# Performance work log

Hardware: AMD Instinct MI355X
Metric: run time of the kernel (lower is better)

## Reference

```python
import jax, jax.numpy as jnp
import numpy as np

N_USERS = 100000
N_ITEMS = 50000
N = N_USERS + N_ITEMS
EMB_DIM = 64
N_LAYERS = 3
NNZ = 6400000
BATCH = 4096


def setup_inputs() -> dict:
    key = jax.random.key(0)
    k = jax.random.split(key, 7)
    user_emb = 0.1 * jax.random.normal(k[0], (N_USERS, EMB_DIM), dtype=jnp.float32)
    item_emb = 0.1 * jax.random.normal(k[1], (N_ITEMS, EMB_DIM), dtype=jnp.float32)
    graph_val = jax.random.uniform(k[2], (NNZ,), dtype=jnp.float32) * 0.05
    graph_src = jax.random.randint(k[3], (NNZ,), 0, N, dtype=jnp.int64) if jax.config.jax_enable_x64 else jax.random.randint(k[3], (NNZ,), 0, N).astype(jnp.int32)
    graph_dst = jax.random.randint(k[4], (NNZ,), 0, N).astype(graph_src.dtype)
    users = jax.random.randint(k[5], (BATCH,), 0, N_USERS).astype(graph_src.dtype)
    items = jax.random.randint(k[6], (BATCH,), 0, N_ITEMS).astype(graph_src.dtype)
    return {"user_emb": user_emb, "item_emb": item_emb, "graph_val": graph_val,
            "graph_src": graph_src, "graph_dst": graph_dst, "users": users, "items": items}


def _spmm(val, src, dst, x):
    # y[src] += val * x[dst]  -- sparse (COO) matrix @ dense
    return jax.ops.segment_sum(val[:, None] * x[dst], src, num_segments=N)


def reference(user_emb, item_emb, graph_val, graph_src, graph_dst, users, items):
    all_emb = jnp.concatenate([user_emb, item_emb], axis=0)  # [N, d]
    acc = all_emb  # running sum over layers (fused mean accumulation)
    x = all_emb
    for _ in range(N_LAYERS):
        x = _spmm(graph_val, graph_src, graph_dst, x)
        acc = acc + x
    light_out = acc / (N_LAYERS + 1)
    all_users = light_out[:N_USERS]
    all_items = light_out[N_USERS:]
    scores = jnp.sum(all_users[users] * all_items[items], axis=1)  # [B]
    return scores
```

## Files before the change

kernel.cpp:

```cpp
#include <hip/hip_runtime.h>


constexpr int N_USERS = 100000;
constexpr int N_ITEMS = 50000;
constexpr int N_NODES = N_USERS + N_ITEMS;
constexpr int EMB = 64;
constexpr int NNZ = 6400000;
constexpr int BATCH = 4096;

constexpr int BSHIFT = 9;
constexpr int BWIDTH = 1 << BSHIFT;
constexpr int NB = (N_NODES + BWIDTH - 1) >> BSHIFT;
constexpr int NBPAD = 512;
constexpr int BSTRIDE = 23500;

constexpr int TILE = 5120;
constexpr int P1_BLOCKS = NNZ / TILE;
constexpr int EPT1 = TILE / 256;

constexpr float QSCALE = 327680.0f;
constexpr float QINV   = 1.0f / 327680.0f;

struct h4 { _Float16 x, y, z, w; };
typedef _Float16 half4v __attribute__((ext_vector_type(4)));

__global__ void gcur_init_kernel(int* __restrict__ gcur) {
    int i = blockIdx.x * blockDim.x + threadIdx.x;
    if (i < NB) gcur[i] = i * BSTRIDE;
}

__global__ void p1_bin_kernel(const int* __restrict__ src, const int* __restrict__ dst,
                              const float* __restrict__ val, int* __restrict__ gcur,
                              uint2* __restrict__ staging) {
    __shared__ int hist[NBPAD];
    __shared__ int gbase[NBPAD];
    __shared__ int cur[NBPAD];
    __shared__ int sbuf[NBPAD];
    __shared__ int lbase[NBPAD];
    __shared__ uint2 ebuf[TILE];
    int t = threadIdx.x;
    int tile = blockIdx.x * TILE;
    int srcs[EPT1];
    #pragma unroll
    for (int k = 0; k < EPT1; ++k) srcs[k] = src[tile + t + k * 256];
    for (int i = t; i < NBPAD; i += 256) { hist[i] = 0; cur[i] = 0; }
    __syncthreads();
    #pragma unroll
    for (int k = 0; k < EPT1; ++k) atomicAdd(&hist[srcs[k] >> BSHIFT], 1);
    __syncthreads();
    for (int i = t; i < NB; i += 256) {
        int h = hist[i];
        gbase[i] = (h > 0) ? atomicAdd(&gcur[i], h) : 0;
    }
    for (int i = t; i < NBPAD; i += 256) sbuf[i] = hist[i];
    __syncthreads();
    int* pin = sbuf; int* pout = lbase;
    for (int off = 1; off < NBPAD; off <<= 1) {
        for (int i = t; i < NBPAD; i += 256) {
            int v = pin[i];
            if (i >= off) v += pin[i - off];
            pout[i] = v;
        }
        __syncthreads();
        int* tmp = pin; pin = pout; pout = tmp;
    }
    for (int i = t; i < NBPAD; i += 256) lbase[i] = pin[i] - hist[i];
    __syncthreads();
    #pragma unroll
    for (int k = 0; k < EPT1; ++k) {
        int i = tile + t + k * 256;
        int s = srcs[k];
        int b = s >> BSHIFT;
        int c = atomicAdd(&cur[b], 1);
        int d = dst[i];
        float v = val[i];
        unsigned q = (unsigned)(v * QSCALE);
        if (q > 16383u) q = 16383u;
        ebuf[lbase[b] + c] = make_uint2((q << 18) | (unsigned)d, (unsigned)s);
    }
    __syncthreads();
    #pragma unroll
    for (int k = 0; k < EPT1; ++k) {
        int j = t + k * 256;
        uint2 e = ebuf[j];
        int b = (int)(e.y >> BSHIFT);
        unsigned pos = (unsigned)(gbase[b] + (j - lbase[b]));
        if (pos < (unsigned)((b + 1) * BSTRIDE))
            staging[pos] = e;
    }
}

__global__ void bucket_scan_kernel(const int* __restrict__ gcur, int* __restrict__ fbase,
                                   int* __restrict__ roff) {
    __shared__ int sA[NBPAD], sB[NBPAD];
    int t = threadIdx.x;
    int c = (t < NB) ? (gcur[t] - t * BSTRIDE) : 0;
    if (c > BSTRIDE) c = BSTRIDE;
    sA[t] = c;
    __syncthreads();
    int* pin = sA; int* pout = sB;
    for (int off = 1; off < NBPAD; off <<= 1) {
        int v = pin[t];
        if (t >= off) v += pin[t - off];
        pout[t] = v;
        __syncthreads();
        int* tmp = pin; pin = pout; pout = tmp;
    }
    if (t < NB) fbase[t] = pin[t] - c;
    if (t == NB - 1) roff[N_NODES] = pin[t];
}

__global__ void p2_sort_kernel(const int* __restrict__ gcur, const int* __restrict__ fbase,
                               const uint2* __restrict__ staging, unsigned* __restrict__ epack,
                               int* __restrict__ roff) {
    __shared__ int hist[BWIDTH], sA[BWIDTH], sB[BWIDTH], cur[BWIDTH];
    int b = blockIdx.x;
    int t = threadIdx.x;
    int cnt = gcur[b] - b * BSTRIDE;
    if (cnt > BSTRIDE) cnt = BSTRIDE;
    int fb = fbase[b];
    int sbase = b * BSTRIDE;
    for (int i = t; i < BWIDTH; i += 256) hist[i] = 0;
    __syncthreads();
    for (int j = t; j < cnt; j += 256) {
        uint2 e = staging[sbase + j];
        atomicAdd(&hist[e.y & (BWIDTH - 1)], 1);
    }
    __syncthreads();
    for (int i = t; i < BWIDTH; i += 256) sA[i] = hist[i];
    __syncthreads();
    int* pin = sA; int* pout = sB;
    for (int off = 1; off < BWIDTH; off <<= 1) {
        for (int i = t; i < BWIDTH; i += 256) {
            int v = pin[i];
            if (i >= off) v += pin[i - off];
            pout[i] = v;
        }
        __syncthreads();
        int* tmp = pin; pin = pout; pout = tmp;
    }
    for (int i = t; i < BWIDTH; i += 256) {
        int excl = pin[i] - hist[i];
        cur[i] = excl;
        int node = (b << BSHIFT) + i;
        if (node < N_NODES) roff[node] = fb + excl;
    }
    __syncthreads();
    for (int j = t; j < cnt; j += 256) {
        uint2 e = staging[sbase + j];
        int p = atomicAdd(&cur[e.y & (BWIDTH - 1)], 1);
        epack[fb + p] = e.x;
    }
}

__global__ void init_kernel(const float4* __restrict__ ue, const float4* __restrict__ ie,
                            h4* __restrict__ x) {
    int i = blockIdx.x * blockDim.x + threadIdx.x;
    const int total = N_NODES * (EMB / 4);
    if (i >= total) return;
    const int usplit = N_USERS * (EMB / 4);
    float4 v = (i < usplit) ? ue[i] : ie[i - usplit];
    x[i] = h4{(_Float16)v.x, (_Float16)v.y, (_Float16)v.z, (_Float16)v.w};
}

__global__ void gather_init_kernel(const float* __restrict__ ue, const float* __restrict__ ie,
                                   const int* __restrict__ users, const int* __restrict__ items,
                                   float* __restrict__ accb) {
    int gid = blockIdx.x * blockDim.x + threadIdx.x;
    int w = gid >> 6;
    int lane = threadIdx.x & 63;
    if (w >= BATCH * 2) return;
    int b = w >> 1;
    float v;
    if (w & 1) v = ie[(long long)items[b] * EMB + lane];
    else       v = ue[(long long)users[b] * EMB + lane];
    accb[(long long)w * EMB + lane] = v;
}

__global__ void gather_add_kernel(const _Float16* __restrict__ x, const int* __restrict__ users,
                                  const int* __restrict__ items, float* __restrict__ accb) {
    int gid = blockIdx.x * blockDim.x + threadIdx.x;
    int w = gid >> 6;
    int lane = threadIdx.x & 63;
    if (w >= BATCH * 2) return;
    int b = w >> 1;
    int node = (w & 1) ? (N_USERS + items[b]) : users[b];
    accb[(long long)w * EMB + lane] += (float)x[(unsigned)node * EMB + lane];
}

__device__ __forceinline__ float dec_val(unsigned e) {
    return ((float)(e >> 18) + 0.5f) * QINV;
}

__device__ __forceinline__ void row_gather_q(int beg, int end, int lane,
                                             const unsigned* __restrict__ epack,
                                             const _Float16* __restrict__ x,
                                             float acc[4]) {
    const int sub = lane >> 4;
    const unsigned li4 = (unsigned)(lane & 15) * 4;
    float a0 = 0, a1 = 0, a2 = 0, a3 = 0;
    float b0 = 0, b1 = 0, b2 = 0, b3 = 0;
    for (int j = beg; j < end; j += 64) {
        int idx = j + lane;
        unsigned e = (idx < end) ? epack[idx] : 0u;
        int cnt = min(64, end - j);
        int t = 0;
        for (; t + 8 <= cnt; t += 8) {
            unsigned eA = __shfl(e, t + sub, 64);
            unsigned eB = __shfl(e, t + 4 + sub, 64);
            half4v hA = *(const half4v*)(x + ((eA & 0x3FFFFu) << 6) + li4);
            half4v hB = *(const half4v*)(x + ((eB & 0x3FFFFu) << 6) + li4);
            float vA = dec_val(eA);
            float vB = dec_val(eB);
            a0 += vA * (float)hA.x;  a1 += vA * (float)hA.y;
            a2 += vA * (float)hA.z;  a3 += vA * (float)hA.w;
            b0 += vB * (float)hB.x;  b1 += vB * (float)hB.y;
            b2 += vB * (float)hB.z;  b3 += vB * (float)hB.w;
        }
        if (t + 4 <= cnt) {
            unsigned eA = __shfl(e, t + sub, 64);
            half4v hA = *(const half4v*)(x + ((eA & 0x3FFFFu) << 6) + li4);
            float vA = dec_val(eA);
            a0 += vA * (float)hA.x;  a1 += vA * (float)hA.y;
            a2 += vA * (float)hA.z;  a3 += vA * (float)hA.w;
            t += 4;
        }
        if (t < cnt) {
            unsigned eA = __shfl(e, t + sub, 64);
            bool ok = (t + sub) < cnt;
            float vA = ok ? dec_val(eA) : 0.0f;
            half4v hA = *(const half4v*)(x + ((eA & 0x3FFFFu) << 6) + li4);
            a0 += vA * (float)hA.x;  a1 += vA * (float)hA.y;
            a2 += vA * (float)hA.z;  a3 += vA * (float)hA.w;
        }
    }
    a0 += b0; a1 += b1; a2 += b2; a3 += b3;
    a0 += __shfl_xor(a0, 16, 64);  a0 += __shfl_xor(a0, 32, 64);
    a1 += __shfl_xor(a1, 16, 64);  a1 += __shfl_xor(a1, 32, 64);
    a2 += __shfl_xor(a2, 16, 64);  a2 += __shfl_xor(a2, 32, 64);
    a3 += __shfl_xor(a3, 16, 64);  a3 += __shfl_xor(a3, 32, 64);
    acc[0] = a0; acc[1] = a1; acc[2] = a2; acc[3] = a3;
}

__global__ void spmm_full_kernel(const int* __restrict__ roff, const unsigned* __restrict__ epack,
                                 const _Float16* __restrict__ x, _Float16* __restrict__ y) {
    int row = blockIdx.x * (blockDim.x >> 6) + (threadIdx.x >> 6);
    int lane = threadIdx.x & 63;
    if (row >= N_NODES) return;
    float acc[4];
    row_gather_q(roff[row], roff[row + 1], lane, epack, x, acc);
    if (lane < 16) {
        half4v h = {(_Float16)acc[0], (_Float16)acc[1], (_Float16)acc[2], (_Float16)acc[3]};
        *(half4v*)(y + ((unsigned)row << 6) + (unsigned)lane * 4) = h;
    }
}

__global__ void spmm_sel_kernel(const int* __restrict__ roff, const unsigned* __restrict__ epack,
                                const _Float16* __restrict__ x, const int* __restrict__ users,
                                const int* __restrict__ items, float* __restrict__ accb) {
    int gid = blockIdx.x * blockDim.x + threadIdx.x;
    int w = gid >> 6;
    int lane = threadIdx.x & 63;
    if (w >= BATCH * 2) return;
    int b = w >> 1;
    int node = (w & 1) ? (N_USERS + items[b]) : users[b];
    float acc[4];
    row_gather_q(roff[node], roff[node + 1], lane, epack, x, acc);
    if (lane < 16) {
        float4* p = (float4*)(accb + ((long long)w << 6) + lane * 4);
        float4 c = *p;
        c.x += acc[0]; c.y += acc[1]; c.z += acc[2]; c.w += acc[3];
        *p = c;
    }
}

__global__ void score_kernel(const float* __restrict__ accb, float* __restrict__ out) {
    int gid = blockIdx.x * blockDim.x + threadIdx.x;
    int b = gid >> 6;
    int lane = threadIdx.x & 63;
    if (b >= BATCH) return;
    float a = accb[(long long)(2 * b) * EMB + lane];
    float c = accb[(long long)(2 * b + 1) * EMB + lane];
    float p = a * c;
    #pragma unroll
    for (int off = 32; off > 0; off >>= 1) p += __shfl_down(p, off, 64);
    if (lane == 0) out[b] = p * (1.0f / 16.0f);
}

extern "C" void kernel_launch(void* const* d_in, const int* in_sizes, int n_in,
                              void* d_out, int out_size, void* d_ws, size_t ws_size,
                              hipStream_t stream) {
    const float* user_emb  = (const float*)d_in[0];
    const float* item_emb  = (const float*)d_in[1];
    const float* graph_val = (const float*)d_in[2];
    const int*   graph_src = (const int*)d_in[3];
    const int*   graph_dst = (const int*)d_in[4];
    const int*   users     = (const int*)d_in[5];
    const int*   items     = (const int*)d_in[6];
    float* out = (float*)d_out;

    char* base = (char*)d_ws;
    const size_t STAGE_BYTES = (size_t)BSTRIDE * NB * 8;
    const size_t XBYTES = (size_t)N_NODES * EMB * 2;
    uint2*    staging = (uint2*)base;
    _Float16* A       = (_Float16*)base;
    _Float16* B       = (_Float16*)(base + XBYTES);
    float*    accb    = (float*)(base + 2 * XBYTES);
    unsigned* epack   = (unsigned*)(base + STAGE_BYTES);
    int*      roff    = (int*)(epack + NNZ);
    int*      gcur    = roff + (N_NODES + 1);
    int*      fbase   = gcur + NB;

    const int totalv4 = N_NODES * (EMB / 4);
    const int vblocks = (totalv4 + 255) / 256;
    const int wblocks = (BATCH * 2 * 64) / 256;
    const int sblocks = (N_NODES + 3) / 4;

    gcur_init_kernel<<<(NB + 255) / 256, 256, 0, stream>>>(gcur);
    p1_bin_kernel<<<P1_BLOCKS, 256, 0, stream>>>(graph_src, graph_dst, graph_val,
                                                 gcur, staging);
    bucket_scan_kernel<<<1, NBPAD, 0, stream>>>(gcur, fbase, roff);
    p2_sort_kernel<<<NB, 256, 0, stream>>>(gcur, fbase, staging, epack, roff);

    init_kernel<<<vblocks, 256, 0, stream>>>((const float4*)user_emb,
                                             (const float4*)item_emb, (h4*)A);
    gather_init_kernel<<<wblocks, 256, 0, stream>>>(user_emb, item_emb, users, items, accb);

    spmm_full_kernel<<<sblocks, 256, 0, stream>>>(roff, epack, A, B);
    gather_add_kernel<<<wblocks, 256, 0, stream>>>(B, users, items, accb);

    spmm_full_kernel<<<sblocks, 256, 0, stream>>>(roff, epack, B, A);
    gather_add_kernel<<<wblocks, 256, 0, stream>>>(A, users, items, accb);

    spmm_sel_kernel<<<wblocks, 256, 0, stream>>>(roff, epack, A, users, items, accb);

    score_kernel<<<(BATCH * 64) / 256, 256, 0, stream>>>(accb, out);
}
```

Baseline: 507.9 us.

## Pad CSR rows to 64-entry windows and drop global bucket scan

Each row's edge list is padded to a multiple of 64 entries inside a fixed per-bucket region, with row offset and window count packed into one word. This removes the single-block bucket scan kernel and lets the SpMM gather loop run fully unrolled with no tail handling, since padding entries are zero (value decodes near zero, index 0). In exchange it adds a large memset of the padded edge buffer and wastes work on padding entries. Zero-padded entries decode to a small nonzero value, so padding slots add a tiny bias from node 0.

```diff
diff --git a/kernel.cpp b/kernel.cpp
--- a/kernel.cpp
+++ b/kernel.cpp
@@ -13,6 +13,7 @@
 constexpr int NB = (N_NODES + BWIDTH - 1) >> BSHIFT;
 constexpr int NBPAD = 512;
 constexpr int BSTRIDE = 23500;
+constexpr int PBSTRIDE = 36864;
 
 constexpr int TILE = 5120;
 constexpr int P1_BLOCKS = NNZ / TILE;
@@ -90,35 +91,13 @@
     }
 }
 
-__global__ void bucket_scan_kernel(const int* __restrict__ gcur, int* __restrict__ fbase,
-                                   int* __restrict__ roff) {
-    __shared__ int sA[NBPAD], sB[NBPAD];
-    int t = threadIdx.x;
-    int c = (t < NB) ? (gcur[t] - t * BSTRIDE) : 0;
-    if (c > BSTRIDE) c = BSTRIDE;
-    sA[t] = c;
-    __syncthreads();
-    int* pin = sA; int* pout = sB;
-    for (int off = 1; off < NBPAD; off <<= 1) {
-        int v = pin[t];
-        if (t >= off) v += pin[t - off];
-        pout[t] = v;
-        __syncthreads();
-        int* tmp = pin; pin = pout; pout = tmp;
-    }
-    if (t < NB) fbase[t] = pin[t] - c;
-    if (t == NB - 1) roff[N_NODES] = pin[t];
-}
-
-__global__ void p2_sort_kernel(const int* __restrict__ gcur, const int* __restrict__ fbase,
-                               const uint2* __restrict__ staging, unsigned* __restrict__ epack,
-                               int* __restrict__ roff) {
+__global__ void p2_sort_kernel(const int* __restrict__ gcur, const uint2* __restrict__ staging,
+                               unsigned* __restrict__ epack, unsigned* __restrict__ prow) {
     __shared__ int hist[BWIDTH], sA[BWIDTH], sB[BWIDTH], cur[BWIDTH];
     int b = blockIdx.x;
     int t = threadIdx.x;
     int cnt = gcur[b] - b * BSTRIDE;
     if (cnt > BSTRIDE) cnt = BSTRIDE;
-    int fb = fbase[b];
     int sbase = b * BSTRIDE;
     for (int i = t; i < BWIDTH; i += 256) hist[i] = 0;
     __syncthreads();
@@ -127,7 +106,7 @@
         atomicAdd(&hist[e.y & (BWIDTH - 1)], 1);
     }
     __syncthreads();
-    for (int i = t; i < BWIDTH; i += 256) sA[i] = hist[i];
+    for (int i = t; i < BWIDTH; i += 256) sA[i] = (hist[i] + 63) >> 6;
     __syncthreads();
     int* pin = sA; int* pout = sB;
     for (int off = 1; off < BWIDTH; off <<= 1) {
@@ -140,16 +119,22 @@
         int* tmp = pin; pin = pout; pout = tmp;
     }
     for (int i = t; i < BWIDTH; i += 256) {
-        int excl = pin[i] - hist[i];
-        cur[i] = excl;
+        int pw = (hist[i] + 63) >> 6;
+        int ps = pin[i] - pw;
+        unsigned poff = (unsigned)(b * PBSTRIDE + 64 * ps);
+        int fit = (PBSTRIDE - 64 * ps) >> 6;
+        if (fit < 0) fit = 0;
+        if (pw > fit) pw = fit;
+        cur[i] = (int)poff;
         int node = (b << BSHIFT) + i;
-        if (node < N_NODES) roff[node] = fb + excl;
-    }
-    __syncthreads();
+        if (node < N_NODES) prow[node] = (poff << 4) | (unsigned)pw;
+    }
+    __syncthreads();
+    unsigned bend = (unsigned)((b + 1) * PBSTRIDE);
     for (int j = t; j < cnt; j += 256) {
         uint2 e = staging[sbase + j];
         int p = atomicAdd(&cur[e.y & (BWIDTH - 1)], 1);
-        epack[fb + p] = e.x;
+        if ((unsigned)p < bend) epack[p] = e.x;
     }
 }
 
@@ -192,7 +177,7 @@
     return ((float)(e >> 18) + 0.5f) * QINV;
 }
 
-__device__ __forceinline__ void row_gather_q(int beg, int end, int lane,
+__device__ __forceinline__ void row_gather_p(unsigned pr, int lane,
                                              const unsigned* __restrict__ epack,
                                              const _Float16* __restrict__ x,
                                              float acc[4]) {
@@ -200,12 +185,13 @@
     const unsigned li4 = (unsigned)(lane & 15) * 4;
     float a0 = 0, a1 = 0, a2 = 0, a3 = 0;
     float b0 = 0, b1 = 0, b2 = 0, b3 = 0;
-    for (int j = beg; j < end; j += 64) {
-        int idx = j + lane;
-        unsigned e = (idx < end) ? epack[idx] : 0u;
-        int cnt = min(64, end - j);
-        int t = 0;
-        for (; t + 8 <= cnt; t += 8) {
+    const unsigned* ep = epack + (pr >> 4);
+    int nwin = (int)(pr & 15u);
+    for (int w = 0; w < nwin; ++w) {
+        unsigned e = ep[lane];
+        ep += 64;
+        #pragma unroll
+        for (int t = 0; t < 64; t += 8) {
             unsigned eA = __shfl(e, t + sub, 64);
             unsigned eB = __shfl(e, t + 4 + sub, 64);
             half4v hA = *(const half4v*)(x + ((eA & 0x3FFFFu) << 6) + li4);
@@ -217,22 +203,6 @@
             b0 += vB * (float)hB.x;  b1 += vB * (float)hB.y;
             b2 += vB * (float)hB.z;  b3 += vB * (float)hB.w;
         }
-        if (t + 4 <= cnt) {
-            unsigned eA = __shfl(e, t + sub, 64);
-            half4v hA = *(const half4v*)(x + ((eA & 0x3FFFFu) << 6) + li4);
-            float vA = dec_val(eA);
-            a0 += vA * (float)hA.x;  a1 += vA * (float)hA.y;
-            a2 += vA * (float)hA.z;  a3 += vA * (float)hA.w;
-            t += 4;
-        }
-        if (t < cnt) {
-            unsigned eA = __shfl(e, t + sub, 64);
-            bool ok = (t + sub) < cnt;
-            float vA = ok ? dec_val(eA) : 0.0f;
-            half4v hA = *(const half4v*)(x + ((eA & 0x3FFFFu) << 6) + li4);
-            a0 += vA * (float)hA.x;  a1 += vA * (float)hA.y;
-            a2 += vA * (float)hA.z;  a3 += vA * (float)hA.w;
-        }
     }
     a0 += b0; a1 += b1; a2 += b2; a3 += b3;
     a0 += __shfl_xor(a0, 16, 64);  a0 += __shfl_xor(a0, 32, 64);
@@ -242,20 +212,22 @@
     acc[0] = a0; acc[1] = a1; acc[2] = a2; acc[3] = a3;
 }
 
-__global__ void spmm_full_kernel(const int* __restrict__ roff, const unsigned* __restrict__ epack,
+__global__ void spmm_full_kernel(const unsigned* __restrict__ prow,
+                                 const unsigned* __restrict__ epack,
                                  const _Float16* __restrict__ x, _Float16* __restrict__ y) {
     int row = blockIdx.x * (blockDim.x >> 6) + (threadIdx.x >> 6);
     int lane = threadIdx.x & 63;
     if (row >= N_NODES) return;
     float acc[4];
-    row_gather_q(roff[row], roff[row + 1], lane, epack, x, acc);
+    row_gather_p(prow[row], lane, epack, x, acc);
     if (lane < 16) {
         half4v h = {(_Float16)acc[0], (_Float16)acc[1], (_Float16)acc[2], (_Float16)acc[3]};
         *(half4v*)(y + ((unsigned)row << 6) + (unsigned)lane * 4) = h;
     }
 }
 
-__global__ void spmm_sel_kernel(const int* __restrict__ roff, const unsigned* __restrict__ epack,
+__global__ void spmm_sel_kernel(const unsigned* __restrict__ prow,
+                                const unsigned* __restrict__ epack,
                                 const _Float16* __restrict__ x, const int* __restrict__ users,
                                 const int* __restrict__ items, float* __restrict__ accb) {
     int gid = blockIdx.x * blockDim.x + threadIdx.x;
@@ -265,7 +237,7 @@
     int b = w >> 1;
     int node = (w & 1) ? (N_USERS + items[b]) : users[b];
     float acc[4];
-    row_gather_q(roff[node], roff[node + 1], lane, epack, x, acc);
+    row_gather_p(prow[node], lane, epack, x, acc);
     if (lane < 16) {
         float4* p = (float4*)(accb + ((long long)w << 6) + lane * 4);
         float4 c = *p;
@@ -302,37 +274,37 @@
     char* base = (char*)d_ws;
     const size_t STAGE_BYTES = (size_t)BSTRIDE * NB * 8;
     const size_t XBYTES = (size_t)N_NODES * EMB * 2;
+    const size_t PB_SLOTS = (size_t)PBSTRIDE * NB;
     uint2*    staging = (uint2*)base;
     _Float16* A       = (_Float16*)base;
     _Float16* B       = (_Float16*)(base + XBYTES);
     float*    accb    = (float*)(base + 2 * XBYTES);
     unsigned* epack   = (unsigned*)(base + STAGE_BYTES);
-    int*      roff    = (int*)(epack + NNZ);
-    int*      gcur    = roff + (N_NODES + 1);
-    int*      fbase   = gcur + NB;
+    unsigned* prow    = epack + PB_SLOTS;
+    int*      gcur    = (int*)(prow + N_NODES);
 
     const int totalv4 = N_NODES * (EMB / 4);
     const int vblocks = (totalv4 + 255) / 256;
     const int wblocks = (BATCH * 2 * 64) / 256;
     const int sblocks = (N_NODES + 3) / 4;
 
+    hipMemsetAsync(epack, 0, PB_SLOTS * sizeof(unsigned), stream);
     gcur_init_kernel<<<(NB + 255) / 256, 256, 0, stream>>>(gcur);
     p1_bin_kernel<<<P1_BLOCKS, 256, 0, stream>>>(graph_src, graph_dst, graph_val,
                                                  gcur, staging);
-    bucket_scan_kernel<<<1, NBPAD, 0, stream>>>(gcur, fbase, roff);
-    p2_sort_kernel<<<NB, 256, 0, stream>>>(gcur, fbase, staging, epack, roff);
+    p2_sort_kernel<<<NB, 256, 0, stream>>>(gcur, staging, epack, prow);
 
     init_kernel<<<vblocks, 256, 0, stream>>>((const float4*)user_emb,
                                              (const float4*)item_emb, (h4*)A);
     gather_init_kernel<<<wblocks, 256, 0, stream>>>(user_emb, item_emb, users, items, accb);
 
-    spmm_full_kernel<<<sblocks, 256, 0, stream>>>(roff, epack, A, B);
+    spmm_full_kernel<<<sblocks, 256, 0, stream>>>(prow, epack, A, B);
     gather_add_kernel<<<wblocks, 256, 0, stream>>>(B, users, items, accb);
 
-    spmm_full_kernel<<<sblocks, 256, 0, stream>>>(roff, epack, B, A);
+    spmm_full_kernel<<<sblocks, 256, 0, stream>>>(prow, epack, B, A);
     gather_add_kernel<<<wblocks, 256, 0, stream>>>(A, users, items, accb);
 
-    spmm_sel_kernel<<<wblocks, 256, 0, stream>>>(roff, epack, A, users, items, accb);
+    spmm_sel_kernel<<<wblocks, 256, 0, stream>>>(prow, epack, A, users, items, accb);
 
     score_kernel<<<(BATCH * 64) / 256, 256, 0, stream>>>(accb, out);
 }
```

New measurement: 504.8 us. Within noise of the previous version (-0.6%).
